# Kernel optimization log

Measured on AMD Instinct MI355X. Metric: run time of the kernel, lower is better.

The kernel has to match this reference:

```python
import jax, jax.numpy as jnp
import numpy as np

N, D_IN, D_HID, D_OUT, ORDER = 8192, 512, 1024, 64, 3

def setup_inputs() -> dict:
    key = jax.random.key(0)
    k = jax.random.split(key, 5)
    x = jax.random.normal(k[0], (N, D_IN), dtype=jnp.float32)
    adj = jax.random.uniform(k[1], (ORDER, N, N), dtype=jnp.float32)
    W1 = jax.random.normal(k[2], (ORDER, D_IN, D_HID), dtype=jnp.float32) * (1.0 / np.sqrt(D_IN))
    b1 = jnp.zeros((D_HID,), dtype=jnp.float32)
    W2 = jax.random.normal(k[3], (ORDER, D_HID, D_OUT), dtype=jnp.float32) * (1.0 / np.sqrt(D_HID))
    b2 = jnp.zeros((D_OUT,), dtype=jnp.float32)
    return {"x": x, "preprocessed": adj, "W1": W1, "b1": b1, "W2": W2, "b2": b2}

def multi_val_gc(x, adj, W, b):
    # x: [N, in], adj: [order, N, N], W: [order, in, out]
    xw = jnp.einsum('ni,kio->kno', x, W)          # [order, N, out]
    out = jnp.einsum('knm,kmo->no', adj, xw)      # sum over orders
    return out + b

def reference(x, preprocessed, W1, b1, W2, b2):
    h = multi_val_gc(x, preprocessed, W1, b1)
    h = jax.nn.relu(h)
    # dropout is identity in eval mode
    h = multi_val_gc(h, preprocessed, W2, b2)
    return jax.nn.log_softmax(h, axis=1)
```

## Files before the change

### kernel.cpp

```cpp
#include <hip/hip_runtime.h>
#include <hip/hip_bf16.h>
#include <cstdint>
#include <cstddef>


typedef __bf16 bf16_t;
typedef __bf16 bf16x8 __attribute__((ext_vector_type(8)));
typedef __bf16 bf16x4 __attribute__((ext_vector_type(4)));
typedef float  f32x4  __attribute__((ext_vector_type(4)));

#define NROWS 8192
#define DIN   512
#define DHID  1024
#define DOUT  64
#define ORD   3
#define KTOT  24576

#define GLDS(g, l) __builtin_amdgcn_global_load_lds( \
    (__attribute__((address_space(1))) void*)(g),    \
    (__attribute__((address_space(3))) void*)(l), 16, 0, 0)


__global__ void k_cvt_x(const float* __restrict__ x, bf16_t* __restrict__ xb) {
  int i = blockIdx.x * blockDim.x + threadIdx.x;
  const float4* p = reinterpret_cast<const float4*>(x) + (size_t)i * 2;
  float4 v0 = p[0], v1 = p[1];
  bf16x8 o;
  o[0]=(bf16_t)v0.x; o[1]=(bf16_t)v0.y; o[2]=(bf16_t)v0.z; o[3]=(bf16_t)v0.w;
  o[4]=(bf16_t)v1.x; o[5]=(bf16_t)v1.y; o[6]=(bf16_t)v1.z; o[7]=(bf16_t)v1.w;
  *reinterpret_cast<bf16x8*>(xb + (size_t)i * 8) = o;
}

__global__ void k_transpose_cvt(const float* __restrict__ src, bf16_t* __restrict__ dst,
                                int R, int C) {
  __shared__ float tile[64][65];
  int ord = blockIdx.z;
  src += (size_t)ord * R * C;
  dst += (size_t)ord * R * C;
  int c0 = blockIdx.x * 64, r0 = blockIdx.y * 64;
  for (int i = 0; i < 16; ++i) {
    int idx = i * 256 + threadIdx.x;
    int r = idx >> 6, c = idx & 63;
    tile[r][c] = src[(size_t)(r0 + r) * C + c0 + c];
  }
  __syncthreads();
  for (int i = 0; i < 16; ++i) {
    int idx = i * 256 + threadIdx.x;
    int cc = idx >> 6, rr = idx & 63;
    dst[(size_t)(c0 + cc) * R + r0 + rr] = (bf16_t)tile[rr][cc];
  }
}

__global__ __launch_bounds__(256) void k_gemm_xw1(
    const bf16_t* __restrict__ xb,
    const bf16_t* __restrict__ w1t,
    bf16_t* __restrict__ xw1t)
{
  __shared__ bf16_t As[128 * 64];
  __shared__ bf16_t Bs[128 * 64];
  int ntile = blockIdx.x, mtile = blockIdx.y, ord = blockIdx.z;
  int tid = threadIdx.x, lane = tid & 63, wid = tid >> 6;
  int wm = wid >> 1, wn = wid & 1;
  int sl = (lane & 7) ^ (lane >> 3);
  f32x4 acc[4][4] = {};
  const bf16_t* w1o = w1t + (size_t)ord * DHID * DIN;
  for (int kt = 0; kt < DIN; kt += 64) {
    for (int j = 0; j < 4; ++j) {
      int q = wid * 4 + j;
      int row = q * 8 + (lane >> 3);
      const bf16_t* g = xb + (size_t)(mtile * 128 + row) * DIN + kt + sl * 8;
      GLDS(g, &As[q * 512]);
    }
    for (int j = 0; j < 4; ++j) {
      int q = wid * 4 + j;
      int row = q * 8 + (lane >> 3);
      const bf16_t* g = w1o + (size_t)(ntile * 128 + row) * DIN + kt + sl * 8;
      GLDS(g, &Bs[q * 512]);
    }
    __syncthreads();
    for (int ks = 0; ks < 2; ++ks) {
      int lsl = (ks << 2) + (lane >> 4);
      int psl = lsl ^ (lane & 7);
      bf16x8 a[4], b[4];
      for (int f = 0; f < 4; ++f)
        a[f] = *reinterpret_cast<const bf16x8*>(&As[(wm * 64 + f * 16 + (lane & 15)) * 64 + psl * 8]);
      for (int f = 0; f < 4; ++f)
        b[f] = *reinterpret_cast<const bf16x8*>(&Bs[(wn * 64 + f * 16 + (lane & 15)) * 64 + psl * 8]);
      for (int fm = 0; fm < 4; ++fm)
        for (int fn = 0; fn < 4; ++fn)
          acc[fm][fn] = __builtin_amdgcn_mfma_f32_16x16x32_bf16(a[fm], b[fn], acc[fm][fn], 0, 0, 0);
    }
    __syncthreads();
  }
  for (int fm = 0; fm < 4; ++fm)
    for (int fn = 0; fn < 4; ++fn) {
      int o  = ntile * 128 + wn * 64 + fn * 16 + (lane & 15);
      int n0 = mtile * 128 + wm * 64 + fm * 16 + ((lane >> 4) << 2);
      bf16x4 v;
      v[0] = (bf16_t)acc[fm][fn][0]; v[1] = (bf16_t)acc[fm][fn][1];
      v[2] = (bf16_t)acc[fm][fn][2]; v[3] = (bf16_t)acc[fm][fn][3];
      *reinterpret_cast<bf16x4*>(&xw1t[(size_t)o * KTOT + ord * NROWS + n0]) = v;
    }
}

__global__ __launch_bounds__(256) void k_gemm_h(
    const float* __restrict__ adj,
    const bf16_t* __restrict__ xw1t,
    const float* __restrict__ b1,
    bf16_t* __restrict__ h)
{
  __shared__ bf16_t As[128 * 64];
  __shared__ bf16_t Bs[128 * 64];
  int d = blockIdx.x;
  int xcd = d & 7;
  int idx = d >> 3;
  int mtile = xcd * 8 + (idx >> 3);
  int ntile = idx & 7;
  int tid = threadIdx.x, lane = tid & 63, wid = tid >> 6;
  int wm = wid >> 1, wn = wid & 1;
  int sl = (lane & 7) ^ (lane >> 3);
  f32x4 acc[4][4] = {};
  for (int kt = 0; kt < KTOT / 64; ++kt) {
    int kk0 = kt * 64;
    int ord = kk0 >> 13;
    int mcol = kk0 & 8191;
    for (int j = 0; j < 4; ++j) {
      int q = wid * 4 + j;
      int row = q * 8 + (lane >> 3);
      const bf16_t* g = xw1t + (size_t)(ntile * 128 + row) * KTOT + kk0 + sl * 8;
      GLDS(g, &Bs[q * 512]);
    }
    const float* abase = adj + (size_t)ord * NROWS * NROWS + (size_t)(mtile * 128) * NROWS + mcol;
    bf16x8 st[4]; int mrow[4], kb[4];
    for (int i = 0; i < 4; ++i) {
      int c = i * 256 + tid;
      mrow[i] = c >> 3; kb[i] = c & 7;
      const float4* p = reinterpret_cast<const float4*>(abase + (size_t)mrow[i] * NROWS + kb[i] * 8);
      float4 v0 = p[0], v1 = p[1];
      bf16x8 o;
      o[0]=(bf16_t)v0.x; o[1]=(bf16_t)v0.y; o[2]=(bf16_t)v0.z; o[3]=(bf16_t)v0.w;
      o[4]=(bf16_t)v1.x; o[5]=(bf16_t)v1.y; o[6]=(bf16_t)v1.z; o[7]=(bf16_t)v1.w;
      st[i] = o;
    }
    for (int i = 0; i < 4; ++i)
      *reinterpret_cast<bf16x8*>(&As[mrow[i] * 64 + (kb[i] ^ (mrow[i] & 7)) * 8]) = st[i];
    __syncthreads();
    for (int ks = 0; ks < 2; ++ks) {
      int lsl = (ks << 2) + (lane >> 4);
      int psl = lsl ^ (lane & 7);
      bf16x8 a[4], b[4];
      for (int f = 0; f < 4; ++f)
        a[f] = *reinterpret_cast<const bf16x8*>(&As[(wm * 64 + f * 16 + (lane & 15)) * 64 + psl * 8]);
      for (int f = 0; f < 4; ++f)
        b[f] = *reinterpret_cast<const bf16x8*>(&Bs[(wn * 64 + f * 16 + (lane & 15)) * 64 + psl * 8]);
      for (int fm = 0; fm < 4; ++fm)
        for (int fn = 0; fn < 4; ++fn)
          acc[fm][fn] = __builtin_amdgcn_mfma_f32_16x16x32_bf16(a[fm], b[fn], acc[fm][fn], 0, 0, 0);
    }
    __syncthreads();
  }
  for (int fm = 0; fm < 4; ++fm)
    for (int fn = 0; fn < 4; ++fn) {
      int o  = ntile * 128 + wn * 64 + fn * 16 + (lane & 15);
      float bias = b1[o];
      int n0 = mtile * 128 + wm * 64 + fm * 16 + ((lane >> 4) << 2);
      for (int j = 0; j < 4; ++j) {
        float v = acc[fm][fn][j] + bias;
        v = v > 0.0f ? v : 0.0f;
        h[(size_t)(n0 + j) * DHID + o] = (bf16_t)v;
      }
    }
}

__global__ __launch_bounds__(256) void k_gemm_xw2(
    const bf16_t* __restrict__ h,
    const bf16_t* __restrict__ w2t,
    bf16_t* __restrict__ xw2t)
{
  __shared__ bf16_t As[128 * 64];
  __shared__ bf16_t Bs[64 * 64];
  int mtile = blockIdx.x, ord = blockIdx.y;
  int tid = threadIdx.x, lane = tid & 63, wid = tid >> 6;
  int wm = wid >> 1, wn = wid & 1;
  int sl = (lane & 7) ^ (lane >> 3);
  f32x4 acc[4][2] = {};
  const bf16_t* w2o = w2t + (size_t)ord * DOUT * DHID;
  for (int kt = 0; kt < DHID; kt += 64) {
    for (int j = 0; j < 4; ++j) {
      int q = wid * 4 + j;
      int row = q * 8 + (lane >> 3);
      const bf16_t* g = h + (size_t)(mtile * 128 + row) * DHID + kt + sl * 8;
      GLDS(g, &As[q * 512]);
    }
    for (int j = 0; j < 2; ++j) {
      int q = wid * 2 + j;
      int row = q * 8 + (lane >> 3);
      const bf16_t* g = w2o + (size_t)row * DHID + kt + sl * 8;
      GLDS(g, &Bs[q * 512]);
    }
    __syncthreads();
    for (int ks = 0; ks < 2; ++ks) {
      int lsl = (ks << 2) + (lane >> 4);
      int psl = lsl ^ (lane & 7);
      bf16x8 a[4], b[2];
      for (int f = 0; f < 4; ++f)
        a[f] = *reinterpret_cast<const bf16x8*>(&As[(wm * 64 + f * 16 + (lane & 15)) * 64 + psl * 8]);
      for (int f = 0; f < 2; ++f)
        b[f] = *reinterpret_cast<const bf16x8*>(&Bs[(wn * 32 + f * 16 + (lane & 15)) * 64 + psl * 8]);
      for (int fm = 0; fm < 4; ++fm)
        for (int fn = 0; fn < 2; ++fn)
          acc[fm][fn] = __builtin_amdgcn_mfma_f32_16x16x32_bf16(a[fm], b[fn], acc[fm][fn], 0, 0, 0);
    }
    __syncthreads();
  }
  for (int fm = 0; fm < 4; ++fm)
    for (int fn = 0; fn < 2; ++fn) {
      int o2 = wn * 32 + fn * 16 + (lane & 15);
      int n0 = mtile * 128 + wm * 64 + fm * 16 + ((lane >> 4) << 2);
      bf16x4 v;
      v[0] = (bf16_t)acc[fm][fn][0]; v[1] = (bf16_t)acc[fm][fn][1];
      v[2] = (bf16_t)acc[fm][fn][2]; v[3] = (bf16_t)acc[fm][fn][3];
      *reinterpret_cast<bf16x4*>(&xw2t[(size_t)o2 * KTOT + ord * NROWS + n0]) = v;
    }
}

__global__ __launch_bounds__(256) void k_gemm_out(
    const float* __restrict__ adj,
    const bf16_t* __restrict__ xw2t,
    float* __restrict__ part)
{
  __shared__ bf16_t As[128 * 64];
  __shared__ bf16_t Bs[64 * 64];
  int mtile = blockIdx.x, ksp = blockIdx.y;
  int tid = threadIdx.x, lane = tid & 63, wid = tid >> 6;
  int wm = wid >> 1, wn = wid & 1;
  int sl = (lane & 7) ^ (lane >> 3);
  f32x4 acc[4][2] = {};
  for (int kt = ksp * 96; kt < ksp * 96 + 96; ++kt) {
    int kk0 = kt * 64;
    int ord = kk0 >> 13;
    int mcol = kk0 & 8191;
    for (int j = 0; j < 2; ++j) {
      int q = wid * 2 + j;
      int row = q * 8 + (lane >> 3);
      const bf16_t* g = xw2t + (size_t)row * KTOT + kk0 + sl * 8;
      GLDS(g, &Bs[q * 512]);
    }
    const float* abase = adj + (size_t)ord * NROWS * NROWS + (size_t)(mtile * 128) * NROWS + mcol;
    bf16x8 st[4]; int mrow[4], kb[4];
    for (int i = 0; i < 4; ++i) {
      int c = i * 256 + tid;
      mrow[i] = c >> 3; kb[i] = c & 7;
      const float4* p = reinterpret_cast<const float4*>(abase + (size_t)mrow[i] * NROWS + kb[i] * 8);
      float4 v0 = p[0], v1 = p[1];
      bf16x8 o;
      o[0]=(bf16_t)v0.x; o[1]=(bf16_t)v0.y; o[2]=(bf16_t)v0.z; o[3]=(bf16_t)v0.w;
      o[4]=(bf16_t)v1.x; o[5]=(bf16_t)v1.y; o[6]=(bf16_t)v1.z; o[7]=(bf16_t)v1.w;
      st[i] = o;
    }
    for (int i = 0; i < 4; ++i)
      *reinterpret_cast<bf16x8*>(&As[mrow[i] * 64 + (kb[i] ^ (mrow[i] & 7)) * 8]) = st[i];
    __syncthreads();
    for (int ks = 0; ks < 2; ++ks) {
      int lsl = (ks << 2) + (lane >> 4);
      int psl = lsl ^ (lane & 7);
      bf16x8 a[4], b[2];
      for (int f = 0; f < 4; ++f)
        a[f] = *reinterpret_cast<const bf16x8*>(&As[(wm * 64 + f * 16 + (lane & 15)) * 64 + psl * 8]);
      for (int f = 0; f < 2; ++f)
        b[f] = *reinterpret_cast<const bf16x8*>(&Bs[(wn * 32 + f * 16 + (lane & 15)) * 64 + psl * 8]);
      for (int fm = 0; fm < 4; ++fm)
        for (int fn = 0; fn < 2; ++fn)
          acc[fm][fn] = __builtin_amdgcn_mfma_f32_16x16x32_bf16(a[fm], b[fn], acc[fm][fn], 0, 0, 0);
    }
    __syncthreads();
  }
  float* pout = part + (size_t)ksp * NROWS * DOUT;
  for (int fm = 0; fm < 4; ++fm)
    for (int fn = 0; fn < 2; ++fn) {
      int o2 = wn * 32 + fn * 16 + (lane & 15);
      int n0 = mtile * 128 + wm * 64 + fm * 16 + ((lane >> 4) << 2);
      for (int j = 0; j < 4; ++j)
        pout[(size_t)(n0 + j) * DOUT + o2] = acc[fm][fn][j];
    }
}

__global__ void k_logsoftmax(const float* __restrict__ part, const float* __restrict__ b2,
                             float* __restrict__ out) {
  int wid = threadIdx.x >> 6, lane = threadIdx.x & 63;
  int n = blockIdx.x * 4 + wid;
  size_t s = (size_t)NROWS * DOUT;
  float v = part[(size_t)n * DOUT + lane] + part[s + (size_t)n * DOUT + lane]
          + part[2 * s + (size_t)n * DOUT + lane] + part[3 * s + (size_t)n * DOUT + lane]
          + b2[lane];
  float mx = v;
  for (int d = 32; d; d >>= 1) mx = fmaxf(mx, __shfl_xor(mx, d));
  float e = expf(v - mx);
  float sum = e;
  for (int d = 32; d; d >>= 1) sum += __shfl_xor(sum, d);
  out[(size_t)n * DOUT + lane] = (v - mx) - logf(sum);
}

extern "C" void kernel_launch(void* const* d_in, const int* in_sizes, int n_in,
                              void* d_out, int out_size, void* d_ws, size_t ws_size,
                              hipStream_t stream) {
  const float* x   = (const float*)d_in[0];
  const float* adj = (const float*)d_in[1];
  const float* W1  = (const float*)d_in[2];
  const float* b1  = (const float*)d_in[3];
  const float* W2  = (const float*)d_in[4];
  const float* b2  = (const float*)d_in[5];
  float* out = (float*)d_out;
  char* ws = (char*)d_ws;

  bf16_t* xb   = (bf16_t*)(ws + 0);
  bf16_t* w1t  = (bf16_t*)(ws + 8388608);
  bf16_t* w2t  = (bf16_t*)(ws + 11534336);
  bf16_t* xw1t = (bf16_t*)(ws + 11927552);
  bf16_t* h    = (bf16_t*)(ws + 62259200);
  bf16_t* xw2t = (bf16_t*)(ws + 79036416);
  float*  part = (float*)(ws + 82182144);

  k_cvt_x<<<2048, 256, 0, stream>>>(x, xb);
  k_transpose_cvt<<<dim3(16, 8, 3), 256, 0, stream>>>(W1, w1t, DIN, DHID);
  k_transpose_cvt<<<dim3(1, 16, 3), 256, 0, stream>>>(W2, w2t, DHID, DOUT);
  k_gemm_xw1<<<dim3(8, 64, 3), 256, 0, stream>>>(xb, w1t, xw1t);
  k_gemm_h<<<512, 256, 0, stream>>>(adj, xw1t, b1, h);
  k_gemm_xw2<<<dim3(64, 3), 256, 0, stream>>>(h, w2t, xw2t);
  k_gemm_out<<<dim3(64, 4), 256, 0, stream>>>(adj, xw2t, part);
  k_logsoftmax<<<2048, 256, 0, stream>>>(part, b2, out);
}
```

Measured before the change: 982.0 us.

## Double-buffer LDS in adjacency GEMMs and double split-K for output GEMM

Both adjacency-streaming GEMMs (k_gemm_h and k_gemm_out) now use double-buffered LDS. The next tile's fp32 adj rows are loaded into registers, and the next B tile is fetched via global_load_lds, while the current tile runs MFMAs, leaving one barrier per iteration. The output GEMM's split-K goes from 4 to 8, giving 512 blocks instead of 256 for better CU coverage. The partial buffer is relocated into the now-dead xw1t region and logsoftmax sums 8 partials. The change doubles LDS per block and adds register pressure, with launch_bounds(256,2) asking the compiler to keep two blocks per CU.

```diff
diff --git a/kernel.cpp b/kernel.cpp
--- a/kernel.cpp
+++ b/kernel.cpp
@@ -79,8 +79,7 @@
     }
     __syncthreads();
     for (int ks = 0; ks < 2; ++ks) {
-      int lsl = (ks << 2) + (lane >> 4);
-      int psl = lsl ^ (lane & 7);
+      int psl = ((ks << 2) + (lane >> 4)) ^ (lane & 7);
       bf16x8 a[4], b[4];
       for (int f = 0; f < 4; ++f)
         a[f] = *reinterpret_cast<const bf16x8*>(&As[(wm * 64 + f * 16 + (lane & 15)) * 64 + psl * 8]);
@@ -103,14 +102,14 @@
     }
 }
 
-__global__ __launch_bounds__(256) void k_gemm_h(
+__global__ __launch_bounds__(256, 2) void k_gemm_h(
     const float* __restrict__ adj,
     const bf16_t* __restrict__ xw1t,
     const float* __restrict__ b1,
     bf16_t* __restrict__ h)
 {
-  __shared__ bf16_t As[128 * 64];
-  __shared__ bf16_t Bs[128 * 64];
+  __shared__ bf16_t As[2][128 * 64];
+  __shared__ bf16_t Bs[2][128 * 64];
   int d = blockIdx.x;
   int xcd = d & 7;
   int idx = d >> 3;
@@ -119,46 +118,97 @@
   int tid = threadIdx.x, lane = tid & 63, wid = tid >> 6;
   int wm = wid >> 1, wn = wid & 1;
   int sl = (lane & 7) ^ (lane >> 3);
+  int mr = tid >> 3, kb = tid & 7;
+  const size_t NN = (size_t)NROWS * NROWS;
   f32x4 acc[4][4] = {};
-  for (int kt = 0; kt < KTOT / 64; ++kt) {
-    int kk0 = kt * 64;
-    int ord = kk0 >> 13;
-    int mcol = kk0 & 8191;
+
+  {
     for (int j = 0; j < 4; ++j) {
       int q = wid * 4 + j;
       int row = q * 8 + (lane >> 3);
-      const bf16_t* g = xw1t + (size_t)(ntile * 128 + row) * KTOT + kk0 + sl * 8;
-      GLDS(g, &Bs[q * 512]);
-    }
-    const float* abase = adj + (size_t)ord * NROWS * NROWS + (size_t)(mtile * 128) * NROWS + mcol;
-    bf16x8 st[4]; int mrow[4], kb[4];
+      GLDS(xw1t + (size_t)(ntile * 128 + row) * KTOT + sl * 8, &Bs[0][q * 512]);
+    }
+    const float* ab = adj + (size_t)(mtile * 128 + mr) * NROWS + kb * 8;
+#pragma unroll
     for (int i = 0; i < 4; ++i) {
-      int c = i * 256 + tid;
-      mrow[i] = c >> 3; kb[i] = c & 7;
-      const float4* p = reinterpret_cast<const float4*>(abase + (size_t)mrow[i] * NROWS + kb[i] * 8);
+      const float4* p = reinterpret_cast<const float4*>(ab + (size_t)(i * 32) * NROWS);
       float4 v0 = p[0], v1 = p[1];
       bf16x8 o;
       o[0]=(bf16_t)v0.x; o[1]=(bf16_t)v0.y; o[2]=(bf16_t)v0.z; o[3]=(bf16_t)v0.w;
       o[4]=(bf16_t)v1.x; o[5]=(bf16_t)v1.y; o[6]=(bf16_t)v1.z; o[7]=(bf16_t)v1.w;
-      st[i] = o;
-    }
-    for (int i = 0; i < 4; ++i)
-      *reinterpret_cast<bf16x8*>(&As[mrow[i] * 64 + (kb[i] ^ (mrow[i] & 7)) * 8]) = st[i];
-    __syncthreads();
+      int row = mr + i * 32;
+      *reinterpret_cast<bf16x8*>(&As[0][row * 64 + (kb ^ (row & 7)) * 8]) = o;
+    }
+  }
+  __syncthreads();
+
+  for (int t = 0; t < KTOT / 64; ++t) {
+    int cur = t & 1;
+    float4 lo0, hi0, lo1, hi1, lo2, hi2, lo3, hi3;
+    bool has_next = (t + 1 < KTOT / 64);
+    if (has_next) {
+      int kk1 = (t + 1) * 64;
+      int ord1 = kk1 >> 13, mcol1 = kk1 & 8191;
+      for (int j = 0; j < 4; ++j) {
+        int q = wid * 4 + j;
+        int row = q * 8 + (lane >> 3);
+        GLDS(xw1t + (size_t)(ntile * 128 + row) * KTOT + kk1 + sl * 8, &Bs[cur ^ 1][q * 512]);
+      }
+      const float* ab = adj + (size_t)ord1 * NN + (size_t)(mtile * 128 + mr) * NROWS + mcol1 + kb * 8;
+      const float4* p0 = reinterpret_cast<const float4*>(ab);
+      const float4* p1 = reinterpret_cast<const float4*>(ab + (size_t)32 * NROWS);
+      const float4* p2 = reinterpret_cast<const float4*>(ab + (size_t)64 * NROWS);
+      const float4* p3 = reinterpret_cast<const float4*>(ab + (size_t)96 * NROWS);
+      lo0 = p0[0]; hi0 = p0[1]; lo1 = p1[0]; hi1 = p1[1];
+      lo2 = p2[0]; hi2 = p2[1]; lo3 = p3[0]; hi3 = p3[1];
+    }
+    const bf16_t* Ac = As[cur];
+    const bf16_t* Bc = Bs[cur];
     for (int ks = 0; ks < 2; ++ks) {
-      int lsl = (ks << 2) + (lane >> 4);
-      int psl = lsl ^ (lane & 7);
+      int psl = ((ks << 2) + (lane >> 4)) ^ (lane & 7);
       bf16x8 a[4], b[4];
       for (int f = 0; f < 4; ++f)
-        a[f] = *reinterpret_cast<const bf16x8*>(&As[(wm * 64 + f * 16 + (lane & 15)) * 64 + psl * 8]);
-      for (int f = 0; f < 4; ++f)
-        b[f] = *reinterpret_cast<const bf16x8*>(&Bs[(wn * 64 + f * 16 + (lane & 15)) * 64 + psl * 8]);
+        a[f] = *reinterpret_cast<const bf16x8*>(&Ac[(wm * 64 + f * 16 + (lane & 15)) * 64 + psl * 8]);
+      for (int f = 0; f < 4; ++f)
+        b[f] = *reinterpret_cast<const bf16x8*>(&Bc[(wn * 64 + f * 16 + (lane & 15)) * 64 + psl * 8]);
       for (int fm = 0; fm < 4; ++fm)
         for (int fn = 0; fn < 4; ++fn)
           acc[fm][fn] = __builtin_amdgcn_mfma_f32_16x16x32_bf16(a[fm], b[fn], acc[fm][fn], 0, 0, 0);
     }
-    __syncthreads();
-  }
+    if (has_next) {
+      bf16_t* An = As[cur ^ 1];
+      {
+        bf16x8 o;
+        o[0]=(bf16_t)lo0.x; o[1]=(bf16_t)lo0.y; o[2]=(bf16_t)lo0.z; o[3]=(bf16_t)lo0.w;
+        o[4]=(bf16_t)hi0.x; o[5]=(bf16_t)hi0.y; o[6]=(bf16_t)hi0.z; o[7]=(bf16_t)hi0.w;
+        int row = mr;
+        *reinterpret_cast<bf16x8*>(&An[row * 64 + (kb ^ (row & 7)) * 8]) = o;
+      }
+      {
+        bf16x8 o;
+        o[0]=(bf16_t)lo1.x; o[1]=(bf16_t)lo1.y; o[2]=(bf16_t)lo1.z; o[3]=(bf16_t)lo1.w;
+        o[4]=(bf16_t)hi1.x; o[5]=(bf16_t)hi1.y; o[6]=(bf16_t)hi1.z; o[7]=(bf16_t)hi1.w;
+        int row = mr + 32;
+        *reinterpret_cast<bf16x8*>(&An[row * 64 + (kb ^ (row & 7)) * 8]) = o;
+      }
+      {
+        bf16x8 o;
+        o[0]=(bf16_t)lo2.x; o[1]=(bf16_t)lo2.y; o[2]=(bf16_t)lo2.z; o[3]=(bf16_t)lo2.w;
+        o[4]=(bf16_t)hi2.x; o[5]=(bf16_t)hi2.y; o[6]=(bf16_t)hi2.z; o[7]=(bf16_t)hi2.w;
+        int row = mr + 64;
+        *reinterpret_cast<bf16x8*>(&An[row * 64 + (kb ^ (row & 7)) * 8]) = o;
+      }
+      {
+        bf16x8 o;
+        o[0]=(bf16_t)lo3.x; o[1]=(bf16_t)lo3.y; o[2]=(bf16_t)lo3.z; o[3]=(bf16_t)lo3.w;
+        o[4]=(bf16_t)hi3.x; o[5]=(bf16_t)hi3.y; o[6]=(bf16_t)hi3.z; o[7]=(bf16_t)hi3.w;
+        int row = mr + 96;
+        *reinterpret_cast<bf16x8*>(&An[row * 64 + (kb ^ (row & 7)) * 8]) = o;
+      }
+      __syncthreads();
+    }
+  }
+
   for (int fm = 0; fm < 4; ++fm)
     for (int fn = 0; fn < 4; ++fn) {
       int o  = ntile * 128 + wn * 64 + fn * 16 + (lane & 15);
@@ -200,8 +250,7 @@
     }
     __syncthreads();
     for (int ks = 0; ks < 2; ++ks) {
-      int lsl = (ks << 2) + (lane >> 4);
-      int psl = lsl ^ (lane & 7);
+      int psl = ((ks << 2) + (lane >> 4)) ^ (lane & 7);
       bf16x8 a[4], b[2];
       for (int f = 0; f < 4; ++f)
         a[f] = *reinterpret_cast<const bf16x8*>(&As[(wm * 64 + f * 16 + (lane & 15)) * 64 + psl * 8]);
@@ -224,57 +273,111 @@
     }
 }
 
-__global__ __launch_bounds__(256) void k_gemm_out(
+__global__ __launch_bounds__(256, 2) void k_gemm_out(
     const float* __restrict__ adj,
     const bf16_t* __restrict__ xw2t,
     float* __restrict__ part)
 {
-  __shared__ bf16_t As[128 * 64];
-  __shared__ bf16_t Bs[64 * 64];
+  __shared__ bf16_t As[2][128 * 64];
+  __shared__ bf16_t Bs[2][64 * 64];
   int mtile = blockIdx.x, ksp = blockIdx.y;
   int tid = threadIdx.x, lane = tid & 63, wid = tid >> 6;
   int wm = wid >> 1, wn = wid & 1;
   int sl = (lane & 7) ^ (lane >> 3);
+  int mr = tid >> 3, kb = tid & 7;
+  const size_t NN = (size_t)NROWS * NROWS;
   f32x4 acc[4][2] = {};
-  for (int kt = ksp * 96; kt < ksp * 96 + 96; ++kt) {
-    int kk0 = kt * 64;
-    int ord = kk0 >> 13;
-    int mcol = kk0 & 8191;
+  const int T0 = ksp * 48, NT = 48;
+
+  {
+    int kk0 = T0 * 64;
+    int ord = kk0 >> 13, mcol = kk0 & 8191;
     for (int j = 0; j < 2; ++j) {
       int q = wid * 2 + j;
       int row = q * 8 + (lane >> 3);
-      const bf16_t* g = xw2t + (size_t)row * KTOT + kk0 + sl * 8;
-      GLDS(g, &Bs[q * 512]);
-    }
-    const float* abase = adj + (size_t)ord * NROWS * NROWS + (size_t)(mtile * 128) * NROWS + mcol;
-    bf16x8 st[4]; int mrow[4], kb[4];
+      GLDS(xw2t + (size_t)row * KTOT + kk0 + sl * 8, &Bs[0][q * 512]);
+    }
+    const float* ab = adj + (size_t)ord * NN + (size_t)(mtile * 128 + mr) * NROWS + mcol + kb * 8;
+#pragma unroll
     for (int i = 0; i < 4; ++i) {
-      int c = i * 256 + tid;
-      mrow[i] = c >> 3; kb[i] = c & 7;
-      const float4* p = reinterpret_cast<const float4*>(abase + (size_t)mrow[i] * NROWS + kb[i] * 8);
+      const float4* p = reinterpret_cast<const float4*>(ab + (size_t)(i * 32) * NROWS);
       float4 v0 = p[0], v1 = p[1];
       bf16x8 o;
       o[0]=(bf16_t)v0.x; o[1]=(bf16_t)v0.y; o[2]=(bf16_t)v0.z; o[3]=(bf16_t)v0.w;
       o[4]=(bf16_t)v1.x; o[5]=(bf16_t)v1.y; o[6]=(bf16_t)v1.z; o[7]=(bf16_t)v1.w;
-      st[i] = o;
-    }
-    for (int i = 0; i < 4; ++i)
-      *reinterpret_cast<bf16x8*>(&As[mrow[i] * 64 + (kb[i] ^ (mrow[i] & 7)) * 8]) = st[i];
-    __syncthreads();
+      int row = mr + i * 32;
+      *reinterpret_cast<bf16x8*>(&As[0][row * 64 + (kb ^ (row & 7)) * 8]) = o;
+    }
+  }
+  __syncthreads();
+
+  for (int t = 0; t < NT; ++t) {
+    int cur = t & 1;
+    float4 lo0, hi0, lo1, hi1, lo2, hi2, lo3, hi3;
+    bool has_next = (t + 1 < NT);
+    if (has_next) {
+      int kk1 = (T0 + t + 1) * 64;
+      int ord1 = kk1 >> 13, mcol1 = kk1 & 8191;
+      for (int j = 0; j < 2; ++j) {
+        int q = wid * 2 + j;
+        int row = q * 8 + (lane >> 3);
+        GLDS(xw2t + (size_t)row * KTOT + kk1 + sl * 8, &Bs[cur ^ 1][q * 512]);
+      }
+      const float* ab = adj + (size_t)ord1 * NN + (size_t)(mtile * 128 + mr) * NROWS + mcol1 + kb * 8;
+      const float4* p0 = reinterpret_cast<const float4*>(ab);
+      const float4* p1 = reinterpret_cast<const float4*>(ab + (size_t)32 * NROWS);
+      const float4* p2 = reinterpret_cast<const float4*>(ab + (size_t)64 * NROWS);
+      const float4* p3 = reinterpret_cast<const float4*>(ab + (size_t)96 * NROWS);
+      lo0 = p0[0]; hi0 = p0[1]; lo1 = p1[0]; hi1 = p1[1];
+      lo2 = p2[0]; hi2 = p2[1]; lo3 = p3[0]; hi3 = p3[1];
+    }
+    const bf16_t* Ac = As[cur];
+    const bf16_t* Bc = Bs[cur];
     for (int ks = 0; ks < 2; ++ks) {
-      int lsl = (ks << 2) + (lane >> 4);
-      int psl = lsl ^ (lane & 7);
+      int psl = ((ks << 2) + (lane >> 4)) ^ (lane & 7);
       bf16x8 a[4], b[2];
       for (int f = 0; f < 4; ++f)
-        a[f] = *reinterpret_cast<const bf16x8*>(&As[(wm * 64 + f * 16 + (lane & 15)) * 64 + psl * 8]);
+        a[f] = *reinterpret_cast<const bf16x8*>(&Ac[(wm * 64 + f * 16 + (lane & 15)) * 64 + psl * 8]);
       for (int f = 0; f < 2; ++f)
-        b[f] = *reinterpret_cast<const bf16x8*>(&Bs[(wn * 32 + f * 16 + (lane & 15)) * 64 + psl * 8]);
+        b[f] = *reinterpret_cast<const bf16x8*>(&Bc[(wn * 32 + f * 16 + (lane & 15)) * 64 + psl * 8]);
       for (int fm = 0; fm < 4; ++fm)
         for (int fn = 0; fn < 2; ++fn)
           acc[fm][fn] = __builtin_amdgcn_mfma_f32_16x16x32_bf16(a[fm], b[fn], acc[fm][fn], 0, 0, 0);
     }
-    __syncthreads();
-  }
+    if (has_next) {
+      bf16_t* An = As[cur ^ 1];
+      {
+        bf16x8 o;
+        o[0]=(bf16_t)lo0.x; o[1]=(bf16_t)lo0.y; o[2]=(bf16_t)lo0.z; o[3]=(bf16_t)lo0.w;
+        o[4]=(bf16_t)hi0.x; o[5]=(bf16_t)hi0.y; o[6]=(bf16_t)hi0.z; o[7]=(bf16_t)hi0.w;
+        int row = mr;
+        *reinterpret_cast<bf16x8*>(&An[row * 64 + (kb ^ (row & 7)) * 8]) = o;
+      }
+      {
+        bf16x8 o;
+        o[0]=(bf16_t)lo1.x; o[1]=(bf16_t)lo1.y; o[2]=(bf16_t)lo1.z; o[3]=(bf16_t)lo1.w;
+        o[4]=(bf16_t)hi1.x; o[5]=(bf16_t)hi1.y; o[6]=(bf16_t)hi1.z; o[7]=(bf16_t)hi1.w;
+        int row = mr + 32;
+        *reinterpret_cast<bf16x8*>(&An[row * 64 + (kb ^ (row & 7)) * 8]) = o;
+      }
+      {
+        bf16x8 o;
+        o[0]=(bf16_t)lo2.x; o[1]=(bf16_t)lo2.y; o[2]=(bf16_t)lo2.z; o[3]=(bf16_t)lo2.w;
+        o[4]=(bf16_t)hi2.x; o[5]=(bf16_t)hi2.y; o[6]=(bf16_t)hi2.z; o[7]=(bf16_t)hi2.w;
+        int row = mr + 64;
+        *reinterpret_cast<bf16x8*>(&An[row * 64 + (kb ^ (row & 7)) * 8]) = o;
+      }
+      {
+        bf16x8 o;
+        o[0]=(bf16_t)lo3.x; o[1]=(bf16_t)lo3.y; o[2]=(bf16_t)lo3.z; o[3]=(bf16_t)lo3.w;
+        o[4]=(bf16_t)hi3.x; o[5]=(bf16_t)hi3.y; o[6]=(bf16_t)hi3.z; o[7]=(bf16_t)hi3.w;
+        int row = mr + 96;
+        *reinterpret_cast<bf16x8*>(&An[row * 64 + (kb ^ (row & 7)) * 8]) = o;
+      }
+      __syncthreads();
+    }
+  }
+
   float* pout = part + (size_t)ksp * NROWS * DOUT;
   for (int fm = 0; fm < 4; ++fm)
     for (int fn = 0; fn < 2; ++fn) {
@@ -290,9 +393,10 @@
   int wid = threadIdx.x >> 6, lane = threadIdx.x & 63;
   int n = blockIdx.x * 4 + wid;
   size_t s = (size_t)NROWS * DOUT;
-  float v = part[(size_t)n * DOUT + lane] + part[s + (size_t)n * DOUT + lane]
-          + part[2 * s + (size_t)n * DOUT + lane] + part[3 * s + (size_t)n * DOUT + lane]
-          + b2[lane];
+  float v = b2[lane];
+#pragma unroll
+  for (int p = 0; p < 8; ++p)
+    v += part[(size_t)p * s + (size_t)n * DOUT + lane];
   float mx = v;
   for (int d = 32; d; d >>= 1) mx = fmaxf(mx, __shfl_xor(mx, d));
   float e = expf(v - mx);
@@ -319,7 +423,7 @@
   bf16_t* xw1t = (bf16_t*)(ws + 11927552);
   bf16_t* h    = (bf16_t*)(ws + 62259200);
   bf16_t* xw2t = (bf16_t*)(ws + 79036416);
-  float*  part = (float*)(ws + 82182144);
+  float*  part = (float*)(ws + 11927552);
 
   k_cvt_x<<<2048, 256, 0, stream>>>(x, xb);
   k_transpose_cvt<<<dim3(16, 8, 3), 256, 0, stream>>>(W1, w1t, DIN, DHID);
@@ -327,6 +431,6 @@
   k_gemm_xw1<<<dim3(8, 64, 3), 256, 0, stream>>>(xb, w1t, xw1t);
   k_gemm_h<<<512, 256, 0, stream>>>(adj, xw1t, b1, h);
   k_gemm_xw2<<<dim3(64, 3), 256, 0, stream>>>(h, w2t, xw2t);
-  k_gemm_out<<<dim3(64, 4), 256, 0, stream>>>(adj, xw2t, part);
+  k_gemm_out<<<dim3(64, 8), 256, 0, stream>>>(adj, xw2t, part);
   k_logsoftmax<<<2048, 256, 0, stream>>>(part, b2, out);
 }
```

New measurement: 1.128 ms. 14.8% more time.

## Pre-convert adjacency to bf16 once and stream it via LDS-direct loads

Applied to the files above, without the earlier changes.

Adds a kernel that converts the fp32 adjacency to bf16 in workspace, then both adjacency GEMMs load it with global_load_lds instead of register-staged fp32 loads and conversion. The output GEMM split-K is raised from 4 to 8 with log-softmax summing 8 partials. The extra conversion pass adds read/write traffic but reduces the bytes read by each GEMM and removes per-tile conversion latency. A fallback path keeps the fp32 kernels when workspace is too small.

```diff
diff --git a/kernel.cpp b/kernel.cpp
--- a/kernel.cpp
+++ b/kernel.cpp
@@ -29,6 +29,20 @@
   o[0]=(bf16_t)v0.x; o[1]=(bf16_t)v0.y; o[2]=(bf16_t)v0.z; o[3]=(bf16_t)v0.w;
   o[4]=(bf16_t)v1.x; o[5]=(bf16_t)v1.y; o[6]=(bf16_t)v1.z; o[7]=(bf16_t)v1.w;
   *reinterpret_cast<bf16x8*>(xb + (size_t)i * 8) = o;
+}
+
+__global__ void k_cvt_adj(const float* __restrict__ a, bf16_t* __restrict__ ab) {
+  size_t i = (size_t)blockIdx.x * blockDim.x + threadIdx.x;
+  const size_t stride = (size_t)gridDim.x * blockDim.x;
+  const float4* src = reinterpret_cast<const float4*>(a);
+#pragma unroll 4
+  for (int it = 0; it < 48; ++it, i += stride) {
+    float4 v0 = src[i * 2], v1 = src[i * 2 + 1];
+    bf16x8 o;
+    o[0]=(bf16_t)v0.x; o[1]=(bf16_t)v0.y; o[2]=(bf16_t)v0.z; o[3]=(bf16_t)v0.w;
+    o[4]=(bf16_t)v1.x; o[5]=(bf16_t)v1.y; o[6]=(bf16_t)v1.z; o[7]=(bf16_t)v1.w;
+    *reinterpret_cast<bf16x8*>(ab + i * 8) = o;
+  }
 }
 
 __global__ void k_transpose_cvt(const float* __restrict__ src, bf16_t* __restrict__ dst,
@@ -68,19 +82,16 @@
     for (int j = 0; j < 4; ++j) {
       int q = wid * 4 + j;
       int row = q * 8 + (lane >> 3);
-      const bf16_t* g = xb + (size_t)(mtile * 128 + row) * DIN + kt + sl * 8;
-      GLDS(g, &As[q * 512]);
-    }
-    for (int j = 0; j < 4; ++j) {
-      int q = wid * 4 + j;
-      int row = q * 8 + (lane >> 3);
-      const bf16_t* g = w1o + (size_t)(ntile * 128 + row) * DIN + kt + sl * 8;
-      GLDS(g, &Bs[q * 512]);
-    }
-    __syncthreads();
-    for (int ks = 0; ks < 2; ++ks) {
-      int lsl = (ks << 2) + (lane >> 4);
-      int psl = lsl ^ (lane & 7);
+      GLDS(xb + (size_t)(mtile * 128 + row) * DIN + kt + sl * 8, &As[q * 512]);
+    }
+    for (int j = 0; j < 4; ++j) {
+      int q = wid * 4 + j;
+      int row = q * 8 + (lane >> 3);
+      GLDS(w1o + (size_t)(ntile * 128 + row) * DIN + kt + sl * 8, &Bs[q * 512]);
+    }
+    __syncthreads();
+    for (int ks = 0; ks < 2; ++ks) {
+      int psl = ((ks << 2) + (lane >> 4)) ^ (lane & 7);
       bf16x8 a[4], b[4];
       for (int f = 0; f < 4; ++f)
         a[f] = *reinterpret_cast<const bf16x8*>(&As[(wm * 64 + f * 16 + (lane & 15)) * 64 + psl * 8]);
@@ -104,7 +115,7 @@
 }
 
 __global__ __launch_bounds__(256) void k_gemm_h(
-    const float* __restrict__ adj,
+    const bf16_t* __restrict__ adjb,
     const bf16_t* __restrict__ xw1t,
     const float* __restrict__ b1,
     bf16_t* __restrict__ h)
@@ -119,16 +130,169 @@
   int tid = threadIdx.x, lane = tid & 63, wid = tid >> 6;
   int wm = wid >> 1, wn = wid & 1;
   int sl = (lane & 7) ^ (lane >> 3);
+  const size_t NN = (size_t)NROWS * NROWS;
+  f32x4 acc[4][4] = {};
+  for (int kt = 0; kt < KTOT / 64; ++kt) {
+    int kk = kt * 64;
+    int ord = kk >> 13, mcol = kk & 8191;
+    const bf16_t* ao = adjb + (size_t)ord * NN + (size_t)(mtile * 128) * NROWS + mcol;
+    for (int j = 0; j < 4; ++j) {
+      int q = wid * 4 + j;
+      int row = q * 8 + (lane >> 3);
+      GLDS(ao + (size_t)row * NROWS + sl * 8, &As[q * 512]);
+    }
+    for (int j = 0; j < 4; ++j) {
+      int q = wid * 4 + j;
+      int row = q * 8 + (lane >> 3);
+      GLDS(xw1t + (size_t)(ntile * 128 + row) * KTOT + kk + sl * 8, &Bs[q * 512]);
+    }
+    __syncthreads();
+    for (int ks = 0; ks < 2; ++ks) {
+      int psl = ((ks << 2) + (lane >> 4)) ^ (lane & 7);
+      bf16x8 a[4], b[4];
+      for (int f = 0; f < 4; ++f)
+        a[f] = *reinterpret_cast<const bf16x8*>(&As[(wm * 64 + f * 16 + (lane & 15)) * 64 + psl * 8]);
+      for (int f = 0; f < 4; ++f)
+        b[f] = *reinterpret_cast<const bf16x8*>(&Bs[(wn * 64 + f * 16 + (lane & 15)) * 64 + psl * 8]);
+      for (int fm = 0; fm < 4; ++fm)
+        for (int fn = 0; fn < 4; ++fn)
+          acc[fm][fn] = __builtin_amdgcn_mfma_f32_16x16x32_bf16(a[fm], b[fn], acc[fm][fn], 0, 0, 0);
+    }
+    __syncthreads();
+  }
+  for (int fm = 0; fm < 4; ++fm)
+    for (int fn = 0; fn < 4; ++fn) {
+      int o  = ntile * 128 + wn * 64 + fn * 16 + (lane & 15);
+      float bias = b1[o];
+      int n0 = mtile * 128 + wm * 64 + fm * 16 + ((lane >> 4) << 2);
+      for (int j = 0; j < 4; ++j) {
+        float v = acc[fm][fn][j] + bias;
+        v = v > 0.0f ? v : 0.0f;
+        h[(size_t)(n0 + j) * DHID + o] = (bf16_t)v;
+      }
+    }
+}
+
+__global__ __launch_bounds__(256) void k_gemm_xw2(
+    const bf16_t* __restrict__ h,
+    const bf16_t* __restrict__ w2t,
+    bf16_t* __restrict__ xw2t)
+{
+  __shared__ bf16_t As[128 * 64];
+  __shared__ bf16_t Bs[64 * 64];
+  int mtile = blockIdx.x, ord = blockIdx.y;
+  int tid = threadIdx.x, lane = tid & 63, wid = tid >> 6;
+  int wm = wid >> 1, wn = wid & 1;
+  int sl = (lane & 7) ^ (lane >> 3);
+  f32x4 acc[4][2] = {};
+  const bf16_t* w2o = w2t + (size_t)ord * DOUT * DHID;
+  for (int kt = 0; kt < DHID; kt += 64) {
+    for (int j = 0; j < 4; ++j) {
+      int q = wid * 4 + j;
+      int row = q * 8 + (lane >> 3);
+      GLDS(h + (size_t)(mtile * 128 + row) * DHID + kt + sl * 8, &As[q * 512]);
+    }
+    for (int j = 0; j < 2; ++j) {
+      int q = wid * 2 + j;
+      int row = q * 8 + (lane >> 3);
+      GLDS(w2o + (size_t)row * DHID + kt + sl * 8, &Bs[q * 512]);
+    }
+    __syncthreads();
+    for (int ks = 0; ks < 2; ++ks) {
+      int psl = ((ks << 2) + (lane >> 4)) ^ (lane & 7);
+      bf16x8 a[4], b[2];
+      for (int f = 0; f < 4; ++f)
+        a[f] = *reinterpret_cast<const bf16x8*>(&As[(wm * 64 + f * 16 + (lane & 15)) * 64 + psl * 8]);
+      for (int f = 0; f < 2; ++f)
+        b[f] = *reinterpret_cast<const bf16x8*>(&Bs[(wn * 32 + f * 16 + (lane & 15)) * 64 + psl * 8]);
+      for (int fm = 0; fm < 4; ++fm)
+        for (int fn = 0; fn < 2; ++fn)
+          acc[fm][fn] = __builtin_amdgcn_mfma_f32_16x16x32_bf16(a[fm], b[fn], acc[fm][fn], 0, 0, 0);
+    }
+    __syncthreads();
+  }
+  for (int fm = 0; fm < 4; ++fm)
+    for (int fn = 0; fn < 2; ++fn) {
+      int o2 = wn * 32 + fn * 16 + (lane & 15);
+      int n0 = mtile * 128 + wm * 64 + fm * 16 + ((lane >> 4) << 2);
+      bf16x4 v;
+      v[0] = (bf16_t)acc[fm][fn][0]; v[1] = (bf16_t)acc[fm][fn][1];
+      v[2] = (bf16_t)acc[fm][fn][2]; v[3] = (bf16_t)acc[fm][fn][3];
+      *reinterpret_cast<bf16x4*>(&xw2t[(size_t)o2 * KTOT + ord * NROWS + n0]) = v;
+    }
+}
+
+__global__ __launch_bounds__(256) void k_gemm_out(
+    const bf16_t* __restrict__ adjb,
+    const bf16_t* __restrict__ xw2t,
+    float* __restrict__ part)
+{
+  __shared__ bf16_t As[128 * 64];
+  __shared__ bf16_t Bs[64 * 64];
+  int mtile = blockIdx.x, ksp = blockIdx.y;
+  int tid = threadIdx.x, lane = tid & 63, wid = tid >> 6;
+  int wm = wid >> 1, wn = wid & 1;
+  int sl = (lane & 7) ^ (lane >> 3);
+  const size_t NN = (size_t)NROWS * NROWS;
+  f32x4 acc[4][2] = {};
+  for (int kt = ksp * 48; kt < ksp * 48 + 48; ++kt) {
+    int kk = kt * 64;
+    int ord = kk >> 13, mcol = kk & 8191;
+    const bf16_t* ao = adjb + (size_t)ord * NN + (size_t)(mtile * 128) * NROWS + mcol;
+    for (int j = 0; j < 4; ++j) {
+      int q = wid * 4 + j;
+      int row = q * 8 + (lane >> 3);
+      GLDS(ao + (size_t)row * NROWS + sl * 8, &As[q * 512]);
+    }
+    for (int j = 0; j < 2; ++j) {
+      int q = wid * 2 + j;
+      int row = q * 8 + (lane >> 3);
+      GLDS(xw2t + (size_t)row * KTOT + kk + sl * 8, &Bs[q * 512]);
+    }
+    __syncthreads();
+    for (int ks = 0; ks < 2; ++ks) {
+      int psl = ((ks << 2) + (lane >> 4)) ^ (lane & 7);
+      bf16x8 a[4], b[2];
+      for (int f = 0; f < 4; ++f)
+        a[f] = *reinterpret_cast<const bf16x8*>(&As[(wm * 64 + f * 16 + (lane & 15)) * 64 + psl * 8]);
+      for (int f = 0; f < 2; ++f)
+        b[f] = *reinterpret_cast<const bf16x8*>(&Bs[(wn * 32 + f * 16 + (lane & 15)) * 64 + psl * 8]);
+      for (int fm = 0; fm < 4; ++fm)
+        for (int fn = 0; fn < 2; ++fn)
+          acc[fm][fn] = __builtin_amdgcn_mfma_f32_16x16x32_bf16(a[fm], b[fn], acc[fm][fn], 0, 0, 0);
+    }
+    __syncthreads();
+  }
+  float* pout = part + (size_t)ksp * NROWS * DOUT;
+  for (int fm = 0; fm < 4; ++fm)
+    for (int fn = 0; fn < 2; ++fn) {
+      int o2 = wn * 32 + fn * 16 + (lane & 15);
+      int n0 = mtile * 128 + wm * 64 + fm * 16 + ((lane >> 4) << 2);
+      for (int j = 0; j < 4; ++j)
+        pout[(size_t)(n0 + j) * DOUT + o2] = acc[fm][fn][j];
+    }
+}
+
+__global__ __launch_bounds__(256) void k_gemm_h_f32(
+    const float* __restrict__ adj, const bf16_t* __restrict__ xw1t,
+    const float* __restrict__ b1, bf16_t* __restrict__ h)
+{
+  __shared__ bf16_t As[128 * 64];
+  __shared__ bf16_t Bs[128 * 64];
+  int d = blockIdx.x;
+  int xcd = d & 7, idx = d >> 3;
+  int mtile = xcd * 8 + (idx >> 3), ntile = idx & 7;
+  int tid = threadIdx.x, lane = tid & 63, wid = tid >> 6;
+  int wm = wid >> 1, wn = wid & 1;
+  int sl = (lane & 7) ^ (lane >> 3);
   f32x4 acc[4][4] = {};
   for (int kt = 0; kt < KTOT / 64; ++kt) {
     int kk0 = kt * 64;
-    int ord = kk0 >> 13;
-    int mcol = kk0 & 8191;
-    for (int j = 0; j < 4; ++j) {
-      int q = wid * 4 + j;
-      int row = q * 8 + (lane >> 3);
-      const bf16_t* g = xw1t + (size_t)(ntile * 128 + row) * KTOT + kk0 + sl * 8;
-      GLDS(g, &Bs[q * 512]);
+    int ord = kk0 >> 13, mcol = kk0 & 8191;
+    for (int j = 0; j < 4; ++j) {
+      int q = wid * 4 + j;
+      int row = q * 8 + (lane >> 3);
+      GLDS(xw1t + (size_t)(ntile * 128 + row) * KTOT + kk0 + sl * 8, &Bs[q * 512]);
     }
     const float* abase = adj + (size_t)ord * NROWS * NROWS + (size_t)(mtile * 128) * NROWS + mcol;
     bf16x8 st[4]; int mrow[4], kb[4];
@@ -146,8 +310,7 @@
       *reinterpret_cast<bf16x8*>(&As[mrow[i] * 64 + (kb[i] ^ (mrow[i] & 7)) * 8]) = st[i];
     __syncthreads();
     for (int ks = 0; ks < 2; ++ks) {
-      int lsl = (ks << 2) + (lane >> 4);
-      int psl = lsl ^ (lane & 7);
+      int psl = ((ks << 2) + (lane >> 4)) ^ (lane & 7);
       bf16x8 a[4], b[4];
       for (int f = 0; f < 4; ++f)
         a[f] = *reinterpret_cast<const bf16x8*>(&As[(wm * 64 + f * 16 + (lane & 15)) * 64 + psl * 8]);
@@ -172,79 +335,24 @@
     }
 }
 
-__global__ __launch_bounds__(256) void k_gemm_xw2(
-    const bf16_t* __restrict__ h,
-    const bf16_t* __restrict__ w2t,
-    bf16_t* __restrict__ xw2t)
+__global__ __launch_bounds__(256) void k_gemm_out_f32(
+    const float* __restrict__ adj, const bf16_t* __restrict__ xw2t,
+    float* __restrict__ part)
 {
   __shared__ bf16_t As[128 * 64];
   __shared__ bf16_t Bs[64 * 64];
-  int mtile = blockIdx.x, ord = blockIdx.y;
+  int mtile = blockIdx.x, ksp = blockIdx.y;
   int tid = threadIdx.x, lane = tid & 63, wid = tid >> 6;
   int wm = wid >> 1, wn = wid & 1;
   int sl = (lane & 7) ^ (lane >> 3);
   f32x4 acc[4][2] = {};
-  const bf16_t* w2o = w2t + (size_t)ord * DOUT * DHID;
-  for (int kt = 0; kt < DHID; kt += 64) {
-    for (int j = 0; j < 4; ++j) {
-      int q = wid * 4 + j;
-      int row = q * 8 + (lane >> 3);
-      const bf16_t* g = h + (size_t)(mtile * 128 + row) * DHID + kt + sl * 8;
-      GLDS(g, &As[q * 512]);
-    }
+  for (int kt = ksp * 48; kt < ksp * 48 + 48; ++kt) {
+    int kk0 = kt * 64;
+    int ord = kk0 >> 13, mcol = kk0 & 8191;
     for (int j = 0; j < 2; ++j) {
       int q = wid * 2 + j;
       int row = q * 8 + (lane >> 3);
-      const bf16_t* g = w2o + (size_t)row * DHID + kt + sl * 8;
-      GLDS(g, &Bs[q * 512]);
-    }
-    __syncthreads();
-    for (int ks = 0; ks < 2; ++ks) {
-      int lsl = (ks << 2) + (lane >> 4);
-      int psl = lsl ^ (lane & 7);
-      bf16x8 a[4], b[2];
-      for (int f = 0; f < 4; ++f)
-        a[f] = *reinterpret_cast<const bf16x8*>(&As[(wm * 64 + f * 16 + (lane & 15)) * 64 + psl * 8]);
-      for (int f = 0; f < 2; ++f)
-        b[f] = *reinterpret_cast<const bf16x8*>(&Bs[(wn * 32 + f * 16 + (lane & 15)) * 64 + psl * 8]);
-      for (int fm = 0; fm < 4; ++fm)
-        for (int fn = 0; fn < 2; ++fn)
-          acc[fm][fn] = __builtin_amdgcn_mfma_f32_16x16x32_bf16(a[fm], b[fn], acc[fm][fn], 0, 0, 0);
-    }
-    __syncthreads();
-  }
-  for (int fm = 0; fm < 4; ++fm)
-    for (int fn = 0; fn < 2; ++fn) {
-      int o2 = wn * 32 + fn * 16 + (lane & 15);
-      int n0 = mtile * 128 + wm * 64 + fm * 16 + ((lane >> 4) << 2);
-      bf16x4 v;
-      v[0] = (bf16_t)acc[fm][fn][0]; v[1] = (bf16_t)acc[fm][fn][1];
-      v[2] = (bf16_t)acc[fm][fn][2]; v[3] = (bf16_t)acc[fm][fn][3];
-      *reinterpret_cast<bf16x4*>(&xw2t[(size_t)o2 * KTOT + ord * NROWS + n0]) = v;
-    }
-}
-
-__global__ __launch_bounds__(256) void k_gemm_out(
-    const float* __restrict__ adj,
-    const bf16_t* __restrict__ xw2t,
-    float* __restrict__ part)
-{
-  __shared__ bf16_t As[128 * 64];
-  __shared__ bf16_t Bs[64 * 64];
-  int mtile = blockIdx.x, ksp = blockIdx.y;
-  int tid = threadIdx.x, lane = tid & 63, wid = tid >> 6;
-  int wm = wid >> 1, wn = wid & 1;
-  int sl = (lane & 7) ^ (lane >> 3);
-  f32x4 acc[4][2] = {};
-  for (int kt = ksp * 96; kt < ksp * 96 + 96; ++kt) {
-    int kk0 = kt * 64;
-    int ord = kk0 >> 13;
-    int mcol = kk0 & 8191;
-    for (int j = 0; j < 2; ++j) {
-      int q = wid * 2 + j;
-      int row = q * 8 + (lane >> 3);
-      const bf16_t* g = xw2t + (size_t)row * KTOT + kk0 + sl * 8;
-      GLDS(g, &Bs[q * 512]);
+      GLDS(xw2t + (size_t)row * KTOT + kk0 + sl * 8, &Bs[q * 512]);
     }
     const float* abase = adj + (size_t)ord * NROWS * NROWS + (size_t)(mtile * 128) * NROWS + mcol;
     bf16x8 st[4]; int mrow[4], kb[4];
@@ -262,8 +370,7 @@
       *reinterpret_cast<bf16x8*>(&As[mrow[i] * 64 + (kb[i] ^ (mrow[i] & 7)) * 8]) = st[i];
     __syncthreads();
     for (int ks = 0; ks < 2; ++ks) {
-      int lsl = (ks << 2) + (lane >> 4);
-      int psl = lsl ^ (lane & 7);
+      int psl = ((ks << 2) + (lane >> 4)) ^ (lane & 7);
       bf16x8 a[4], b[2];
       for (int f = 0; f < 4; ++f)
         a[f] = *reinterpret_cast<const bf16x8*>(&As[(wm * 64 + f * 16 + (lane & 15)) * 64 + psl * 8]);
@@ -290,9 +397,10 @@
   int wid = threadIdx.x >> 6, lane = threadIdx.x & 63;
   int n = blockIdx.x * 4 + wid;
   size_t s = (size_t)NROWS * DOUT;
-  float v = part[(size_t)n * DOUT + lane] + part[s + (size_t)n * DOUT + lane]
-          + part[2 * s + (size_t)n * DOUT + lane] + part[3 * s + (size_t)n * DOUT + lane]
-          + b2[lane];
+  float v = b2[lane];
+#pragma unroll
+  for (int p = 0; p < 8; ++p)
+    v += part[(size_t)p * s + (size_t)n * DOUT + lane];
   float mx = v;
   for (int d = 32; d; d >>= 1) mx = fmaxf(mx, __shfl_xor(mx, d));
   float e = expf(v - mx);
@@ -313,20 +421,44 @@
   float* out = (float*)d_out;
   char* ws = (char*)d_ws;
 
-  bf16_t* xb   = (bf16_t*)(ws + 0);
-  bf16_t* w1t  = (bf16_t*)(ws + 8388608);
-  bf16_t* w2t  = (bf16_t*)(ws + 11534336);
-  bf16_t* xw1t = (bf16_t*)(ws + 11927552);
-  bf16_t* h    = (bf16_t*)(ws + 62259200);
-  bf16_t* xw2t = (bf16_t*)(ws + 79036416);
-  float*  part = (float*)(ws + 82182144);
-
-  k_cvt_x<<<2048, 256, 0, stream>>>(x, xb);
-  k_transpose_cvt<<<dim3(16, 8, 3), 256, 0, stream>>>(W1, w1t, DIN, DHID);
-  k_transpose_cvt<<<dim3(1, 16, 3), 256, 0, stream>>>(W2, w2t, DHID, DOUT);
-  k_gemm_xw1<<<dim3(8, 64, 3), 256, 0, stream>>>(xb, w1t, xw1t);
-  k_gemm_h<<<512, 256, 0, stream>>>(adj, xw1t, b1, h);
-  k_gemm_xw2<<<dim3(64, 3), 256, 0, stream>>>(h, w2t, xw2t);
-  k_gemm_out<<<dim3(64, 4), 256, 0, stream>>>(adj, xw2t, part);
-  k_logsoftmax<<<2048, 256, 0, stream>>>(part, b2, out);
-}
+  const size_t ADJB_SZ = 402653184ULL;
+  const size_t NEED    = 484835328ULL;
+
+  if (ws_size >= NEED) {
+    bf16_t* adjb = (bf16_t*)(ws + 0);
+    bf16_t* xb   = (bf16_t*)(ws + ADJB_SZ);
+    bf16_t* w1t  = (bf16_t*)(ws + ADJB_SZ + 8388608);
+    bf16_t* w2t  = (bf16_t*)(ws + ADJB_SZ + 11534336);
+    bf16_t* xw1t = (bf16_t*)(ws + ADJB_SZ + 11927552);
+    bf16_t* h    = (bf16_t*)(ws + ADJB_SZ + 62259200);
+    bf16_t* xw2t = (bf16_t*)(ws + ADJB_SZ + 79036416);
+    float*  part = (float*)(ws + ADJB_SZ + 11927552);
+
+    k_cvt_adj<<<2048, 256, 0, stream>>>(adj, adjb);
+    k_cvt_x<<<2048, 256, 0, stream>>>(x, xb);
+    k_transpose_cvt<<<dim3(16, 8, 3), 256, 0, stream>>>(W1, w1t, DIN, DHID);
+    k_transpose_cvt<<<dim3(1, 16, 3), 256, 0, stream>>>(W2, w2t, DHID, DOUT);
+    k_gemm_xw1<<<dim3(8, 64, 3), 256, 0, stream>>>(xb, w1t, xw1t);
+    k_gemm_h<<<512, 256, 0, stream>>>(adjb, xw1t, b1, h);
+    k_gemm_xw2<<<dim3(64, 3), 256, 0, stream>>>(h, w2t, xw2t);
+    k_gemm_out<<<dim3(64, 8), 256, 0, stream>>>(adjb, xw2t, part);
+    k_logsoftmax<<<2048, 256, 0, stream>>>(part, b2, out);
+  } else {
+    bf16_t* xb   = (bf16_t*)(ws + 0);
+    bf16_t* w1t  = (bf16_t*)(ws + 8388608);
+    bf16_t* w2t  = (bf16_t*)(ws + 11534336);
+    bf16_t* xw1t = (bf16_t*)(ws + 11927552);
+    bf16_t* h    = (bf16_t*)(ws + 62259200);
+    bf16_t* xw2t = (bf16_t*)(ws + 79036416);
+    float*  part = (float*)(ws + 11927552);
+
+    k_cvt_x<<<2048, 256, 0, stream>>>(x, xb);
+    k_transpose_cvt<<<dim3(16, 8, 3), 256, 0, stream>>>(W1, w1t, DIN, DHID);
+    k_transpose_cvt<<<dim3(1, 16, 3), 256, 0, stream>>>(W2, w2t, DHID, DOUT);
+    k_gemm_xw1<<<dim3(8, 64, 3), 256, 0, stream>>>(xb, w1t, xw1t);
+    k_gemm_h_f32<<<512, 256, 0, stream>>>(adj, xw1t, b1, h);
+    k_gemm_xw2<<<dim3(64, 3), 256, 0, stream>>>(h, w2t, xw2t);
+    k_gemm_out_f32<<<dim3(64, 8), 256, 0, stream>>>(adj, xw2t, part);
+    k_logsoftmax<<<2048, 256, 0, stream>>>(part, b2, out);
+  }
+}
```

Result: faster. 942.4 us (-4.0%).
